# Optimization experiments

Hardware: AMD Instinct MI355X
Metric: run time of the kernel (lower is better)

The kernel has to match this reference:

```python
import jax, jax.numpy as jnp
import numpy as np

N, E, B = 100000, 1000000, 64
DIN, DS, H, NG = 128, 1024, 256, 20


def setup_inputs() -> dict:
    key = jax.random.key(0)
    ks = jax.random.split(key, 48)
    lin = lambda k, i, o: (jax.random.normal(k, (i, o), jnp.float32) / np.sqrt(i)).astype(jnp.float32)
    inp = {
        'x': jax.random.normal(ks[0], (N, DIN), jnp.float32),
        'edge_index': jax.random.randint(ks[1], (2, E), 0, N, jnp.int32),
        'batch': jnp.sort(jax.random.randint(ks[2], (N,), 0, B, jnp.int32)),
        'static_features': jax.random.normal(ks[3], (B, DS), jnp.float32),
        'temporal_feats': jax.random.normal(ks[4], (B, 5), jnp.float32),
        'type_idx': jax.random.randint(ks[5], (B,), 0, 10, jnp.int32),
        'type_emb': jax.random.normal(ks[6], (10, H), jnp.float32),
        # static encoder
        'Ws1': lin(ks[7], DS, H), 'bs1': jnp.zeros(H), 'Ws2': lin(ks[8], H, H), 'bs2': jnp.zeros(H),
        # 3 GCN convs
        'Wc1': lin(ks[9], DIN, H), 'bc1': jnp.zeros(H),
        'Wc2': lin(ks[10], H, H), 'bc2': jnp.zeros(H),
        'Wc3': lin(ks[11], H, H), 'bc3': jnp.zeros(H),
        # residual dim_match linears
        'Wd1': lin(ks[12], DIN, H), 'bd1': jnp.zeros(H),
        'Wd2': lin(ks[13], H, H), 'bd2': jnp.zeros(H),
        'Wd3': lin(ks[14], H, H), 'bd3': jnp.zeros(H),
        # temporal MLP (5 -> H//2 -> H)
        'Wt1': lin(ks[15], 5, H // 2), 'bt1': jnp.zeros(H // 2),
        'Wt2': lin(ks[16], H // 2, H), 'bt2': jnp.zeros(H),
        # pattern detector
        'Wp1': lin(ks[17], H, H // 2), 'bp1': jnp.zeros(H // 2),
        'Wp2': lin(ks[18], H // 2, H), 'bp2': jnp.zeros(H),
        # fusion (5H -> 2H -> H)
        'Wf1': lin(ks[19], 5 * H, 2 * H), 'bf1': jnp.zeros(2 * H),
        'Wf2': lin(ks[20], 2 * H, H), 'bf2': jnp.zeros(H),
        # heads
        'Wg': lin(ks[21], H, NG), 'bg': jnp.zeros(NG),
        'Wtp': lin(ks[22], H, 1), 'btp': jnp.zeros(1),
    }
    return inp


def reference(x, edge_index, batch, static_features, temporal_feats, type_idx, type_emb,
              Ws1, bs1, Ws2, bs2,
              Wc1, bc1, Wc2, bc2, Wc3, bc3,
              Wd1, bd1, Wd2, bd2, Wd3, bd3,
              Wt1, bt1, Wt2, bt2,
              Wp1, bp1, Wp2, bp2,
              Wf1, bf1, Wf2, bf2,
              Wg, bg, Wtp, btp):
    n = x.shape[0]
    b = static_features.shape[0]
    src, dst = edge_index[0], edge_index[1]
    # GCN symmetric norm with self-loops: deg = 1 + in-degree
    deg = 1.0 + jax.ops.segment_sum(jnp.ones(src.shape[0], x.dtype), dst, num_segments=n)
    dinv = deg ** -0.5
    ew = dinv[src] * dinv[dst]  # [E] edge norm weights

    def gcn(h_in, W, bias):
        h = h_in @ W  # [n, H]
        agg = jax.ops.segment_sum(h[src] * ew[:, None], dst, num_segments=n)
        return agg + h / deg[:, None] + bias  # neighbor agg + self-loop + bias

    # 3 GCN layers with residual dim_match (dropout is identity at inference)
    x1 = jax.nn.relu(gcn(x, Wc1, bc1)) + (x @ Wd1 + bd1)
    x2 = jax.nn.relu(gcn(x1, Wc2, bc2)) + (x1 @ Wd2 + bd2)
    x3 = jax.nn.relu(gcn(x2, Wc3, bc3)) + (x2 @ Wd3 + bd3)

    pat = jax.nn.relu(jax.nn.relu(x3 @ Wp1 + bp1) @ Wp2 + bp2)

    counts = jnp.maximum(jax.ops.segment_sum(jnp.ones(n, x.dtype), batch, num_segments=b), 1.0)
    graph_embed = jax.ops.segment_sum(x3, batch, num_segments=b) / counts[:, None]
    pattern_embed = jax.ops.segment_sum(pat, batch, num_segments=b) / counts[:, None]

    static_embed = jax.nn.relu(static_features @ Ws1 + bs1) @ Ws2 + bs2
    temporal_embed = jax.nn.relu(temporal_feats @ Wt1 + bt1) @ Wt2 + bt2
    type_embed = type_emb[type_idx]

    combined = jnp.concatenate([graph_embed, static_embed, temporal_embed, type_embed, pattern_embed], axis=1)
    fused = jax.nn.relu(combined @ Wf1 + bf1) @ Wf2 + bf2
    group_logits = fused @ Wg + bg
    time_pred = fused @ Wtp + btp
    return fused, group_logits, time_pred
```

## Files before the change

### kernel.cpp

```cpp
#include <hip/hip_runtime.h>

#define H 256
#define LDK 40

typedef __attribute__((ext_vector_type(8))) short bf16x8;
typedef __attribute__((ext_vector_type(4))) float f32x4;

__device__ __forceinline__ float b2f(ushort h) {
    return __uint_as_float(((unsigned)h) << 16);
}
__device__ __forceinline__ ushort f2bf(float f) {
    unsigned u = __float_as_uint(f);
    unsigned r = (u + 0x7FFF + ((u >> 16) & 1)) >> 16;
    return (ushort)r;
}

__global__ __launch_bounds__(256) void k_zero2_i(int* p, int* q, int n) {
    int i = blockIdx.x * 256 + threadIdx.x;
    if (i < n) { p[i] = 0; q[i] = 0; }
}

__global__ __launch_bounds__(256) void k_zero_f(float* p, int n) {
    int i = blockIdx.x * 256 + threadIdx.x;
    if (i < n) p[i] = 0.f;
}

__global__ __launch_bounds__(256) void k_count_deg_i(const int* __restrict__ dst, int* cnt, int E) {
    int i = blockIdx.x * 256 + threadIdx.x;
    if (i < E) atomicAdd(&cnt[dst[i]], 1);
}

__global__ __launch_bounds__(256) void k_scan1(const int* __restrict__ cnt, int* __restrict__ partial,
                                               int* __restrict__ bsums, int N) {
    __shared__ int s[256];
    int t = threadIdx.x;
    int idx = blockIdx.x * 256 + t;
    int v = idx < N ? cnt[idx] : 0;
    s[t] = v;
    __syncthreads();
    for (int off = 1; off < 256; off <<= 1) {
        int add = (t >= off) ? s[t - off] : 0;
        __syncthreads();
        s[t] += add;
        __syncthreads();
    }
    if (idx < N) partial[idx] = s[t];
    if (t == 255) bsums[blockIdx.x] = s[t];
}

__global__ __launch_bounds__(1024) void k_scan2(int* bsums, int nb) {
    __shared__ int s[1024];
    int t = threadIdx.x;
    s[t] = (t < nb) ? bsums[t] : 0;
    __syncthreads();
    for (int off = 1; off < 1024; off <<= 1) {
        int add = (t >= off) ? s[t - off] : 0;
        __syncthreads();
        s[t] += add;
        __syncthreads();
    }
    if (t < nb) bsums[t] = s[t];
}

__global__ __launch_bounds__(256) void k_scan3(const int* __restrict__ partial, const int* __restrict__ bsums,
                                               const int* __restrict__ cnt,
                                               int* __restrict__ rowptr, float* __restrict__ dinv,
                                               float* __restrict__ selfw, int N) {
    int idx = blockIdx.x * 256 + threadIdx.x;
    if (idx < N) {
        int off = blockIdx.x > 0 ? bsums[blockIdx.x - 1] : 0;
        rowptr[idx + 1] = partial[idx] + off;
        if (idx == 0) rowptr[0] = 0;
        float d = 1.0f + (float)cnt[idx];
        dinv[idx] = rsqrtf(d);
        selfw[idx] = 1.0f / d;
    }
}

__global__ __launch_bounds__(256) void k_scatter(const int* __restrict__ src, const int* __restrict__ dst,
                                                 const float* __restrict__ dinv, const int* __restrict__ rowptr,
                                                 int* __restrict__ fill, int* __restrict__ esrc,
                                                 float* __restrict__ ewt, int E) {
    int e = blockIdx.x * 256 + threadIdx.x;
    if (e >= E) return;
    int s = src[e], d = dst[e];
    int pos = rowptr[d] + atomicAdd(&fill[d], 1);
    esrc[pos] = s;
    ewt[pos] = dinv[s] * dinv[d];
}

__device__ __forceinline__ void tcvt_one(long i, const float* __restrict__ W, ushort* __restrict__ Wt,
                                         int K, int M) {
    int k = (int)(i / M), m = (int)(i - (long)k * M);
    Wt[(size_t)m * K + k] = f2bf(W[(size_t)k * M + m]);
}

__global__ __launch_bounds__(256) void k_prep(
    const float* __restrict__ x, ushort* __restrict__ xh, long nx, int DIN,
    const float* __restrict__ Wc1, ushort* Wc1t, const float* __restrict__ Wd1, ushort* Wd1t,
    const float* __restrict__ Wc2, ushort* Wc2t, const float* __restrict__ Wd2, ushort* Wd2t,
    const float* __restrict__ Wc3, ushort* Wc3t, const float* __restrict__ Wd3, ushort* Wd3t,
    const float* __restrict__ Wp1, ushort* Wp1t, const float* __restrict__ Wp2, ushort* Wp2t) {
    long i = (long)blockIdx.x * 256 + threadIdx.x;
    if (i < nx) { xh[i] = f2bf(x[i]); return; }
    i -= nx;
    long n1 = (long)DIN * 256;
    if (i < n1) { tcvt_one(i, Wc1, Wc1t, DIN, 256); return; }
    i -= n1;
    if (i < n1) { tcvt_one(i, Wd1, Wd1t, DIN, 256); return; }
    i -= n1;
    if (i < 65536) { tcvt_one(i, Wc2, Wc2t, 256, 256); return; }
    i -= 65536;
    if (i < 65536) { tcvt_one(i, Wd2, Wd2t, 256, 256); return; }
    i -= 65536;
    if (i < 65536) { tcvt_one(i, Wc3, Wc3t, 256, 256); return; }
    i -= 65536;
    if (i < 65536) { tcvt_one(i, Wd3, Wd3t, 256, 256); return; }
    i -= 65536;
    if (i < 32768) { tcvt_one(i, Wp1, Wp1t, 256, 128); return; }
    i -= 32768;
    if (i < 32768) { tcvt_one(i, Wp2, Wp2t, 128, 256); return; }
}

__global__ __launch_bounds__(256) void k_gather_b4(const ushort* __restrict__ xin, const int* __restrict__ rowptr,
                                                   const int* __restrict__ esrc, const float* __restrict__ ewt,
                                                   const float* __restrict__ selfw, ushort* __restrict__ p,
                                                   int N, int SX, int SP) {
    int node = blockIdx.x * 4 + (threadIdx.x >> 6);
    if (node >= N) return;
    int c = (threadIdx.x & 63) << 2;
    ushort4 h = *(const ushort4*)(xin + (size_t)node * SX + c);
    float sw = selfw[node];
    float a0 = b2f(h.x) * sw, a1 = b2f(h.y) * sw, a2 = b2f(h.z) * sw, a3 = b2f(h.w) * sw;
    int j = rowptr[node], r1 = rowptr[node + 1];
    for (; j + 3 < r1; j += 4) {
        int s0 = esrc[j], s1 = esrc[j + 1], s2 = esrc[j + 2], s3 = esrc[j + 3];
        float w0 = ewt[j], w1 = ewt[j + 1], w2 = ewt[j + 2], w3 = ewt[j + 3];
        ushort4 v0 = *(const ushort4*)(xin + (size_t)s0 * SX + c);
        ushort4 v1 = *(const ushort4*)(xin + (size_t)s1 * SX + c);
        ushort4 v2 = *(const ushort4*)(xin + (size_t)s2 * SX + c);
        ushort4 v3 = *(const ushort4*)(xin + (size_t)s3 * SX + c);
        a0 += b2f(v0.x) * w0 + b2f(v1.x) * w1 + b2f(v2.x) * w2 + b2f(v3.x) * w3;
        a1 += b2f(v0.y) * w0 + b2f(v1.y) * w1 + b2f(v2.y) * w2 + b2f(v3.y) * w3;
        a2 += b2f(v0.z) * w0 + b2f(v1.z) * w1 + b2f(v2.z) * w2 + b2f(v3.z) * w3;
        a3 += b2f(v0.w) * w0 + b2f(v1.w) * w1 + b2f(v2.w) * w2 + b2f(v3.w) * w3;
    }
    for (; j < r1; ++j) {
        int s0 = esrc[j];
        float w0 = ewt[j];
        ushort4 v0 = *(const ushort4*)(xin + (size_t)s0 * SX + c);
        a0 += b2f(v0.x) * w0; a1 += b2f(v0.y) * w0; a2 += b2f(v0.z) * w0; a3 += b2f(v0.w) * w0;
    }
    ushort4 o;
    o.x = f2bf(a0); o.y = f2bf(a1); o.z = f2bf(a2); o.w = f2bf(a3);
    *(ushort4*)(p + (size_t)node * SP + c) = o;
}

__global__ __launch_bounds__(256) void k_gather_b2(const ushort* __restrict__ xin, const int* __restrict__ rowptr,
                                                   const int* __restrict__ esrc, const float* __restrict__ ewt,
                                                   const float* __restrict__ selfw, ushort* __restrict__ p,
                                                   int N, int SX, int SP) {
    int node = blockIdx.x * 4 + (threadIdx.x >> 6);
    if (node >= N) return;
    int c = (threadIdx.x & 63) << 1;
    ushort2 h = *(const ushort2*)(xin + (size_t)node * SX + c);
    float sw = selfw[node];
    float a0 = b2f(h.x) * sw, a1 = b2f(h.y) * sw;
    int j = rowptr[node], r1 = rowptr[node + 1];
    for (; j + 3 < r1; j += 4) {
        int s0 = esrc[j], s1 = esrc[j + 1], s2 = esrc[j + 2], s3 = esrc[j + 3];
        float w0 = ewt[j], w1 = ewt[j + 1], w2 = ewt[j + 2], w3 = ewt[j + 3];
        ushort2 v0 = *(const ushort2*)(xin + (size_t)s0 * SX + c);
        ushort2 v1 = *(const ushort2*)(xin + (size_t)s1 * SX + c);
        ushort2 v2 = *(const ushort2*)(xin + (size_t)s2 * SX + c);
        ushort2 v3 = *(const ushort2*)(xin + (size_t)s3 * SX + c);
        a0 += b2f(v0.x) * w0 + b2f(v1.x) * w1 + b2f(v2.x) * w2 + b2f(v3.x) * w3;
        a1 += b2f(v0.y) * w0 + b2f(v1.y) * w1 + b2f(v2.y) * w2 + b2f(v3.y) * w3;
    }
    for (; j < r1; ++j) {
        int s0 = esrc[j];
        float w0 = ewt[j];
        ushort2 v0 = *(const ushort2*)(xin + (size_t)s0 * SX + c);
        a0 += b2f(v0.x) * w0; a1 += b2f(v0.y) * w0;
    }
    ushort2 o;
    o.x = f2bf(a0); o.y = f2bf(a1);
    *(ushort2*)(p + (size_t)node * SP + c) = o;
}

__global__ __launch_bounds__(256, 2) void k_fused_mfma(
    const ushort* __restrict__ Pm, const ushort* __restrict__ X,
    const ushort* __restrict__ Wct, const ushort* __restrict__ Wdt,
    const float* __restrict__ bc, const float* __restrict__ bd,
    ushort* __restrict__ Out, int N, int K, int SP, int SX) {
    __shared__ short Ps[64 * LDK];
    __shared__ short Xs[64 * LDK];
    __shared__ short Wcs[256 * LDK];
    __shared__ short Wds[256 * LDK];
    const int tid = threadIdx.x;
    const int wave = tid >> 6, lane = tid & 63;
    const int row0 = blockIdx.x * 64;

    f32x4 accC[4][4], accD[4][4];
#pragma unroll
    for (int i = 0; i < 4; ++i)
#pragma unroll
        for (int j = 0; j < 4; ++j) { accC[i][j] = (f32x4)0.f; accD[i][j] = (f32x4)0.f; }

    const int sr = tid >> 2, sc = (tid & 3) * 8;
    int grow = row0 + sr; if (grow > N - 1) grow = N - 1;
    const int m = lane & 15, kh = (lane >> 4) * 8;

    for (int k0 = 0; k0 < K; k0 += 32) {
        *(uint4*)&Ps[sr * LDK + sc] = *(const uint4*)(Pm + (size_t)grow * SP + k0 + sc);
        *(uint4*)&Xs[sr * LDK + sc] = *(const uint4*)(X + (size_t)grow * SX + k0 + sc);
#pragma unroll
        for (int p = 0; p < 4; ++p) {
            int col = p * 64 + (tid >> 2);
            *(uint4*)&Wcs[col * LDK + sc] = *(const uint4*)(Wct + (size_t)col * K + k0 + sc);
            *(uint4*)&Wds[col * LDK + sc] = *(const uint4*)(Wdt + (size_t)col * K + k0 + sc);
        }
        __syncthreads();
        bf16x8 aP[4], aX[4], bC[4], bD[4];
#pragma unroll
        for (int i = 0; i < 4; ++i) {
            aP[i] = *(bf16x8*)&Ps[(16 * i + m) * LDK + kh];
            aX[i] = *(bf16x8*)&Xs[(16 * i + m) * LDK + kh];
        }
#pragma unroll
        for (int j = 0; j < 4; ++j) {
            int c = wave * 64 + 16 * j + m;
            bC[j] = *(bf16x8*)&Wcs[c * LDK + kh];
            bD[j] = *(bf16x8*)&Wds[c * LDK + kh];
        }
#pragma unroll
        for (int i = 0; i < 4; ++i)
#pragma unroll
            for (int j = 0; j < 4; ++j) {
                accC[i][j] = __builtin_amdgcn_mfma_f32_16x16x32_bf16(aP[i], bC[j], accC[i][j], 0, 0, 0);
                accD[i][j] = __builtin_amdgcn_mfma_f32_16x16x32_bf16(aX[i], bD[j], accD[i][j], 0, 0, 0);
            }
        __syncthreads();
    }

    const int rq = (lane >> 4) * 4;
#pragma unroll
    for (int j = 0; j < 4; ++j) {
        int col = wave * 64 + 16 * j + m;
        float bcv = bc[col], bdv = bd[col];
#pragma unroll
        for (int i = 0; i < 4; ++i)
#pragma unroll
            for (int g = 0; g < 4; ++g) {
                int row = row0 + 16 * i + rq + g;
                if (row < N) {
                    float v = fmaxf(accC[i][j][g] + bcv, 0.f) + accD[i][j][g] + bdv;
                    Out[(size_t)row * 256 + col] = f2bf(v);
                }
            }
    }
}

__global__ __launch_bounds__(256, 2) void k_gemm_mfma(
    const ushort* __restrict__ A, const ushort* __restrict__ Wt, const float* __restrict__ bias,
    ushort* __restrict__ Out, int N, int K, int M, int SA, int dorelu) {
    __shared__ short As[128 * LDK];
    __shared__ short Wls[256 * LDK];
    const int tid = threadIdx.x;
    const int wave = tid >> 6, lane = tid & 63;
    const int MW = M >> 6;
    const int R = 16384 / M;
    const int row0 = blockIdx.x * R;
    const int row_off = (wave / MW) * 64, col_off = (wave % MW) * 64;

    f32x4 acc[4][4];
#pragma unroll
    for (int i = 0; i < 4; ++i)
#pragma unroll
        for (int j = 0; j < 4; ++j) acc[i][j] = (f32x4)0.f;

    const int m = lane & 15, kh = (lane >> 4) * 8, sc = (tid & 3) * 8;

    for (int k0 = 0; k0 < K; k0 += 32) {
        for (int c = tid; c < R * 4; c += 256) {
            int r = c >> 2, ck = (c & 3) * 8;
            int gr = row0 + r; if (gr > N - 1) gr = N - 1;
            *(uint4*)&As[r * LDK + ck] = *(const uint4*)(A + (size_t)gr * SA + k0 + ck);
        }
        for (int p = 0; p < MW; ++p) {
            int col = p * 64 + (tid >> 2);
            *(uint4*)&Wls[col * LDK + sc] = *(const uint4*)(Wt + (size_t)col * K + k0 + sc);
        }
        __syncthreads();
        bf16x8 af[4], bf[4];
#pragma unroll
        for (int i = 0; i < 4; ++i) af[i] = *(bf16x8*)&As[(row_off + 16 * i + m) * LDK + kh];
#pragma unroll
        for (int j = 0; j < 4; ++j) bf[j] = *(bf16x8*)&Wls[(col_off + 16 * j + m) * LDK + kh];
#pragma unroll
        for (int i = 0; i < 4; ++i)
#pragma unroll
            for (int j = 0; j < 4; ++j)
                acc[i][j] = __builtin_amdgcn_mfma_f32_16x16x32_bf16(af[i], bf[j], acc[i][j], 0, 0, 0);
        __syncthreads();
    }

    const int rq = (lane >> 4) * 4;
#pragma unroll
    for (int j = 0; j < 4; ++j) {
        int col = col_off + 16 * j + m;
        float bv = bias[col];
#pragma unroll
        for (int i = 0; i < 4; ++i)
#pragma unroll
            for (int g = 0; g < 4; ++g) {
                int row = row0 + row_off + 16 * i + rq + g;
                if (row < N) {
                    float v = acc[i][j][g] + bv;
                    if (dorelu) v = fmaxf(v, 0.f);
                    Out[(size_t)row * M + col] = f2bf(v);
                }
            }
    }
}

__global__ __launch_bounds__(256, 2) void k_pat2_pool(
    const ushort* __restrict__ A, const ushort* __restrict__ Wt, const float* __restrict__ bias,
    const int* __restrict__ batch, float* __restrict__ pesum, int N, int K, int SA) {
    __shared__ short As[64 * LDK];
    __shared__ short Wls[256 * LDK];
    __shared__ int sbatch[64];
    const int tid = threadIdx.x;
    const int wave = tid >> 6, lane = tid & 63;
    const int row0 = blockIdx.x * 64;
    const int col_off = wave * 64;

    f32x4 acc[4][4];
#pragma unroll
    for (int i = 0; i < 4; ++i)
#pragma unroll
        for (int j = 0; j < 4; ++j) acc[i][j] = (f32x4)0.f;

    const int m = lane & 15, kh = (lane >> 4) * 8, sc = (tid & 3) * 8;
    if (tid < 64) {
        int r = row0 + tid;
        sbatch[tid] = batch[r < N ? r : (N - 1)];
    }

    for (int k0 = 0; k0 < K; k0 += 32) {
        {
            int r = tid >> 2, ck = (tid & 3) * 8;
            int gr = row0 + r; if (gr > N - 1) gr = N - 1;
            *(uint4*)&As[r * LDK + ck] = *(const uint4*)(A + (size_t)gr * SA + k0 + ck);
        }
#pragma unroll
        for (int p = 0; p < 4; ++p) {
            int col = p * 64 + (tid >> 2);
            *(uint4*)&Wls[col * LDK + sc] = *(const uint4*)(Wt + (size_t)col * K + k0 + sc);
        }
        __syncthreads();
        bf16x8 af[4], bf[4];
#pragma unroll
        for (int i = 0; i < 4; ++i) af[i] = *(bf16x8*)&As[(16 * i + m) * LDK + kh];
#pragma unroll
        for (int j = 0; j < 4; ++j) bf[j] = *(bf16x8*)&Wls[(col_off + 16 * j + m) * LDK + kh];
#pragma unroll
        for (int i = 0; i < 4; ++i)
#pragma unroll
            for (int j = 0; j < 4; ++j)
                acc[i][j] = __builtin_amdgcn_mfma_f32_16x16x32_bf16(af[i], bf[j], acc[i][j], 0, 0, 0);
        __syncthreads();
    }

    const int rq = (lane >> 4) * 4;
    const int g0 = sbatch[0];
    const int g1 = sbatch[63];
    for (int g = g0; g <= g1; ++g) {
#pragma unroll
        for (int j = 0; j < 4; ++j) {
            float bv = bias[col_off + 16 * j + m];
            float s = 0.f;
#pragma unroll
            for (int i = 0; i < 4; ++i)
#pragma unroll
                for (int q = 0; q < 4; ++q) {
                    int rl = 16 * i + rq + q;
                    bool ok = (sbatch[rl] == g) && (row0 + rl < N);
                    float v = fmaxf(acc[i][j][q] + bv, 0.f);
                    s += ok ? v : 0.f;
                }
            s += __shfl_down(s, 32, 64);
            s += __shfl_down(s, 16, 64);
            if (lane < 16) atomicAdd(&pesum[(size_t)g * 256 + col_off + 16 * j + lane], s);
        }
    }
}

__global__ void k_ranges(const int* __restrict__ batch, int N, int B, int* __restrict__ start,
                         float* __restrict__ countsf) {
    int b = threadIdx.x;
    if (b <= B) {
        int lo = 0, hi = N;
        while (lo < hi) {
            int mid = (lo + hi) >> 1;
            if (batch[mid] < b) lo = mid + 1; else hi = mid;
        }
        start[b] = lo;
    }
    __syncthreads();
    if (b < B) {
        int cnt = start[b + 1] - start[b];
        countsf[b] = (float)(cnt > 0 ? cnt : 1);
    }
}

#define POOLS 16
__global__ __launch_bounds__(256) void k_pool2(const ushort* __restrict__ M_, const int* __restrict__ start,
                                               float* __restrict__ outsum) {
    int b = blockIdx.x;
    int s = blockIdx.y;
    int wave = threadIdx.x >> 6, lane = threadIdx.x & 63;
    int r0 = start[b], r1 = start[b + 1];
    int stripe = s * 4 + wave;
    float a0 = 0.f, a1 = 0.f, a2 = 0.f, a3 = 0.f;
    for (int r = r0 + stripe; r < r1; r += POOLS * 4) {
        ushort4 v = *(const ushort4*)(M_ + (size_t)r * 256 + lane * 4);
        a0 += b2f(v.x); a1 += b2f(v.y); a2 += b2f(v.z); a3 += b2f(v.w);
    }
    __shared__ float red[4][256];
    *(float4*)&red[wave][lane * 4] = make_float4(a0, a1, a2, a3);
    __syncthreads();
    int col = threadIdx.x;
    float t = red[0][col] + red[1][col] + red[2][col] + red[3][col];
    if (t != 0.f) atomicAdd(&outsum[(size_t)b * 256 + col], t);
}

__global__ __launch_bounds__(256) void k_fin_comb(const float* __restrict__ gesum, const float* __restrict__ pesum,
                                                  const float* __restrict__ countsf,
                                                  const float* __restrict__ temb, const int* __restrict__ tidx,
                                                  float* __restrict__ comb) {
    int b = blockIdx.x, t = threadIdx.x;
    float inv = 1.0f / countsf[b];
    float* o = comb + (size_t)b * 1280;
    o[t] = gesum[(size_t)b * 256 + t] * inv;
    o[768 + t] = temb[(size_t)tidx[b] * 256 + t];
    o[1024 + t] = pesum[(size_t)b * 256 + t] * inv;
}

__global__ __launch_bounds__(256) void k_dense(const float* __restrict__ vin, int vs,
                                               const float* __restrict__ W, const float* __restrict__ bias,
                                               float* __restrict__ out, int os, int oo,
                                               int K, int M, int relu) {
    const int b = blockIdx.y;
    const int wave = threadIdx.x >> 6, lane = threadIdx.x & 63;
    const int c = blockIdx.x * 64 + lane;
    const float* vrow = vin + (size_t)b * vs;
    float acc = 0.f;
    int k = wave;
    for (; k + 28 < K; k += 32) {
#pragma unroll
        for (int u = 0; u < 8; ++u)
            acc += vrow[k + 4 * u] * W[(size_t)(k + 4 * u) * M + c];
    }
    for (; k < K; k += 4)
        acc += vrow[k] * W[(size_t)k * M + c];
    __shared__ float red[4][64];
    red[wave][lane] = acc;
    __syncthreads();
    if (wave == 0) {
        float s = red[0][lane] + red[1][lane] + red[2][lane] + red[3][lane] + bias[c];
        if (relu) s = fmaxf(s, 0.f);
        out[(size_t)b * os + oo + c] = s;
    }
}

__global__ __launch_bounds__(256) void k_heads_small(const float* __restrict__ fused,
                                                     const float* __restrict__ Wg, const float* __restrict__ bg,
                                                     const float* __restrict__ Wtp, const float* __restrict__ btp,
                                                     float* __restrict__ out_logits, float* __restrict__ out_tp,
                                                     int NG) {
    __shared__ float lf[256];
    int b = blockIdx.x, tid = threadIdx.x;
    int wave = tid >> 6, lane = tid & 63;
    lf[tid] = fused[(size_t)b * 256 + tid];
    __syncthreads();
    for (int c = wave; c < NG; c += 4) {
        float s = 0.f;
#pragma unroll
        for (int k = lane; k < 256; k += 64) s += lf[k] * Wg[(size_t)k * NG + c];
#pragma unroll
        for (int off = 32; off > 0; off >>= 1) s += __shfl_down(s, off, 64);
        if (lane == 0) out_logits[(size_t)b * NG + c] = s + bg[c];
    }
    if (wave == 0) {
        float s = 0.f;
#pragma unroll
        for (int k = lane; k < 256; k += 64) s += lf[k] * Wtp[k];
#pragma unroll
        for (int off = 32; off > 0; off >>= 1) s += __shfl_down(s, off, 64);
        if (lane == 0) out_tp[b] = s + btp[0];
    }
}

extern "C" void kernel_launch(void* const* d_in, const int* in_sizes, int n_in,
                              void* d_out, int out_size, void* d_ws, size_t ws_size,
                              hipStream_t stream) {
    const float* x   = (const float*)d_in[0];
    const int* ei    = (const int*)d_in[1];
    const int* batch = (const int*)d_in[2];
    const float* sf  = (const float*)d_in[3];
    const float* tf  = (const float*)d_in[4];
    const int* tidx  = (const int*)d_in[5];
    const float* temb = (const float*)d_in[6];
    const float *Ws1 = (const float*)d_in[7],  *bs1 = (const float*)d_in[8];
    const float *Ws2 = (const float*)d_in[9],  *bs2 = (const float*)d_in[10];
    const float *Wc1 = (const float*)d_in[11], *bc1 = (const float*)d_in[12];
    const float *Wc2 = (const float*)d_in[13], *bc2 = (const float*)d_in[14];
    const float *Wc3 = (const float*)d_in[15], *bc3 = (const float*)d_in[16];
    const float *Wd1 = (const float*)d_in[17], *bd1 = (const float*)d_in[18];
    const float *Wd2 = (const float*)d_in[19], *bd2 = (const float*)d_in[20];
    const float *Wd3 = (const float*)d_in[21], *bd3 = (const float*)d_in[22];
    const float *Wt1 = (const float*)d_in[23], *bt1 = (const float*)d_in[24];
    const float *Wt2 = (const float*)d_in[25], *bt2 = (const float*)d_in[26];
    const float *Wp1 = (const float*)d_in[27], *bp1 = (const float*)d_in[28];
    const float *Wp2 = (const float*)d_in[29], *bp2 = (const float*)d_in[30];
    const float *Wf1 = (const float*)d_in[31], *bf1 = (const float*)d_in[32];
    const float *Wf2 = (const float*)d_in[33], *bf2 = (const float*)d_in[34];
    const float *Wg  = (const float*)d_in[35], *bg  = (const float*)d_in[36];
    const float *Wtp = (const float*)d_in[37], *btp = (const float*)d_in[38];

    const int N = in_sizes[2];
    const int E = in_sizes[1] / 2;
    const int B = in_sizes[5];
    const int DIN = in_sizes[0] / N;
    const int DS = in_sizes[3] / B;
    const int NG = in_sizes[36];
    const int* src = ei;
    const int* dst = ei + E;

    char* w = (char*)d_ws;
    ushort* A   = (ushort*)w;              w += (size_t)N * 256 * 2;
    ushort* Bb  = (ushort*)w;              w += (size_t)N * 256 * 2;
    ushort* xh  = (ushort*)w;              w += (size_t)N * 128 * 2;
    ushort* Wc1t = (ushort*)w;             w += 128 * 256 * 2;
    ushort* Wd1t = (ushort*)w;             w += 128 * 256 * 2;
    ushort* Wc2t = (ushort*)w;             w += 256 * 256 * 2;
    ushort* Wd2t = (ushort*)w;             w += 256 * 256 * 2;
    ushort* Wc3t = (ushort*)w;             w += 256 * 256 * 2;
    ushort* Wd3t = (ushort*)w;             w += 256 * 256 * 2;
    ushort* Wp1t = (ushort*)w;             w += 256 * 128 * 2;
    ushort* Wp2t = (ushort*)w;             w += 128 * 256 * 2;
    int* esrc   = (int*)w;                 w += (size_t)E * 4;
    float* ewt  = (float*)w;               w += (size_t)E * 4;
    int* cnt    = (int*)w;                 w += (size_t)N * 4;
    int* part   = (int*)w;                 w += (size_t)N * 4;
    int* rowptr = (int*)w;                 w += (size_t)(N + 1) * 4;
    int* fill   = (int*)w;                 w += (size_t)N * 4;
    int* bsums  = (int*)w;                 w += 1024 * 4;
    float* dinv = (float*)w;               w += (size_t)N * 4;
    float* selfw = (float*)w;              w += (size_t)N * 4;
    int* startp = (int*)w;                 w += (B + 1) * 4;
    float* countsf = (float*)w;            w += B * 4;
    float* ge = (float*)w;                 w += B * 256 * 4;
    float* pe = (float*)w;                 w += B * 256 * 4;
    float* s1buf = (float*)w;              w += B * 256 * 4;
    float* t1buf = (float*)w;              w += B * 128 * 4;
    float* comb = (float*)w;               w += B * 1280 * 4;
    float* fh = (float*)w;                 w += B * 512 * 4;

    float* out_fused = (float*)d_out;
    float* out_logits = out_fused + (size_t)B * H;
    float* out_tp = out_logits + (size_t)B * NG;

    dim3 blk(256);
    const int nbN = (N + 255) / 256;
    const int nbE = (E + 255) / 256;

    k_zero2_i<<<dim3(nbN), blk, 0, stream>>>(cnt, fill, N);
    k_count_deg_i<<<dim3(nbE), blk, 0, stream>>>(dst, cnt, E);
    k_scan1<<<dim3(nbN), blk, 0, stream>>>(cnt, part, bsums, N);
    k_scan2<<<dim3(1), dim3(1024), 0, stream>>>(bsums, nbN);
    k_scan3<<<dim3(nbN), blk, 0, stream>>>(part, bsums, cnt, rowptr, dinv, selfw, N);
    k_scatter<<<dim3(nbE), blk, 0, stream>>>(src, dst, dinv, rowptr, fill, esrc, ewt, E);

    {
        long nx = (long)N * DIN;
        long tot = nx + 2L * DIN * 256 + 4L * 65536 + 2L * 32768;
        k_prep<<<dim3((unsigned)((tot + 255) / 256)), blk, 0, stream>>>(
            x, xh, nx, DIN, Wc1, Wc1t, Wd1, Wd1t, Wc2, Wc2t, Wd2, Wd2t,
            Wc3, Wc3t, Wd3, Wd3t, Wp1, Wp1t, Wp2, Wp2t);
        k_ranges<<<dim3(1), dim3(128), 0, stream>>>(batch, N, B, startp, countsf);
        k_zero_f<<<dim3((2 * B * 256 + 255) / 256), blk, 0, stream>>>(ge, 2 * B * 256);
    }

    const int ngb = (N + 3) / 4;
    const int nfb = (N + 63) / 64;

    k_dense<<<dim3(4, B), blk, 0, stream>>>(sf, DS, Ws1, bs1, s1buf, 256, 0, DS, 256, 1);
    k_dense<<<dim3(4, B), blk, 0, stream>>>(s1buf, 256, Ws2, bs2, comb, 1280, 256, 256, 256, 0);
    k_dense<<<dim3(2, B), blk, 0, stream>>>(tf, 5, Wt1, bt1, t1buf, 128, 0, 5, 128, 1);
    k_dense<<<dim3(4, B), blk, 0, stream>>>(t1buf, 128, Wt2, bt2, comb, 1280, 512, 128, 256, 0);

    k_gather_b2<<<dim3(ngb), blk, 0, stream>>>(xh, rowptr, esrc, ewt, selfw, A, N, 128, 128);
    k_fused_mfma<<<dim3(nfb), blk, 0, stream>>>(A, xh, Wc1t, Wd1t, bc1, bd1, Bb, N, 128, 128, 128);
    k_gather_b4<<<dim3(ngb), blk, 0, stream>>>(Bb, rowptr, esrc, ewt, selfw, A, N, 256, 256);
    k_fused_mfma<<<dim3(nfb), blk, 0, stream>>>(A, Bb, Wc2t, Wd2t, bc2, bd2, A, N, 256, 256, 256);
    k_gather_b4<<<dim3(ngb), blk, 0, stream>>>(A, rowptr, esrc, ewt, selfw, Bb, N, 256, 256);
    k_fused_mfma<<<dim3(nfb), blk, 0, stream>>>(Bb, A, Wc3t, Wd3t, bc3, bd3, Bb, N, 256, 256, 256);

    k_pool2<<<dim3(B, POOLS), blk, 0, stream>>>(Bb, startp, ge);
    k_gemm_mfma<<<dim3((N + 127) / 128), blk, 0, stream>>>(Bb, Wp1t, bp1, A, N, 256, 128, 256, 1);
    k_pat2_pool<<<dim3((N + 63) / 64), blk, 0, stream>>>(A, Wp2t, bp2, batch, pe, N, 128, 128);
    k_fin_comb<<<dim3(B), blk, 0, stream>>>(ge, pe, countsf, temb, tidx, comb);

    k_dense<<<dim3(8, B), blk, 0, stream>>>(comb, 1280, Wf1, bf1, fh, 512, 0, 1280, 512, 1);
    k_dense<<<dim3(4, B), blk, 0, stream>>>(fh, 512, Wf2, bf2, out_fused, 256, 0, 512, 256, 0);
    k_heads_small<<<dim3(B), blk, 0, stream>>>(out_fused, Wg, bg, Wtp, btp, out_logits, out_tp, NG);
}
```

Measured before the change: 871.9 us.

## Use direct global-to-LDS loads with XOR swizzle and K=64 tiles in fused GCN GEMM

The fused conv+residual MFMA kernel now stages tiles with global_load_lds (buffer-to-LDS DMA) instead of loading through registers, doubles the K tile from 32 to 64, and replaces row padding with an XOR swizzle on the 16-byte chunk index to avoid LDS bank conflicts. This targets VGPR pressure and load/store instruction overhead in the staging phase and halves the number of barriers per K. LDS use rises to about 80KB per block, which may reduce occupancy below the two blocks per CU requested by the launch bounds. It also requires K to be a multiple of 64.

```diff
diff --git a/kernel.cpp b/kernel.cpp
--- a/kernel.cpp
+++ b/kernel.cpp
@@ -13,6 +13,12 @@
     unsigned u = __float_as_uint(f);
     unsigned r = (u + 0x7FFF + ((u >> 16) & 1)) >> 16;
     return (ushort)r;
+}
+
+__device__ __forceinline__ void gload16(const ushort* g, const short* l) {
+    __builtin_amdgcn_global_load_lds(
+        (const __attribute__((address_space(1))) void*)(const void*)g,
+        (__attribute__((address_space(3))) void*)(void*)l, 16, 0, 0);
 }
 
 __global__ __launch_bounds__(256) void k_zero2_i(int* p, int* q, int n) {
@@ -193,10 +199,10 @@
     const ushort* __restrict__ Wct, const ushort* __restrict__ Wdt,
     const float* __restrict__ bc, const float* __restrict__ bd,
     ushort* __restrict__ Out, int N, int K, int SP, int SX) {
-    __shared__ short Ps[64 * LDK];
-    __shared__ short Xs[64 * LDK];
-    __shared__ short Wcs[256 * LDK];
-    __shared__ short Wds[256 * LDK];
+    __shared__ __align__(16) short Ps[64 * 64];
+    __shared__ __align__(16) short Xs[64 * 64];
+    __shared__ __align__(16) short Wcs[256 * 64];
+    __shared__ __align__(16) short Wds[256 * 64];
     const int tid = threadIdx.x;
     const int wave = tid >> 6, lane = tid & 63;
     const int row0 = blockIdx.x * 64;
@@ -207,43 +213,57 @@
 #pragma unroll
         for (int j = 0; j < 4; ++j) { accC[i][j] = (f32x4)0.f; accD[i][j] = (f32x4)0.f; }
 
-    const int sr = tid >> 2, sc = (tid & 3) * 8;
-    int grow = row0 + sr; if (grow > N - 1) grow = N - 1;
-    const int m = lane & 15, kh = (lane >> 4) * 8;
-
-    for (int k0 = 0; k0 < K; k0 += 32) {
-        *(uint4*)&Ps[sr * LDK + sc] = *(const uint4*)(Pm + (size_t)grow * SP + k0 + sc);
-        *(uint4*)&Xs[sr * LDK + sc] = *(const uint4*)(X + (size_t)grow * SX + k0 + sc);
-#pragma unroll
-        for (int p = 0; p < 4; ++p) {
-            int col = p * 64 + (tid >> 2);
-            *(uint4*)&Wcs[col * LDK + sc] = *(const uint4*)(Wct + (size_t)col * K + k0 + sc);
-            *(uint4*)&Wds[col * LDK + sc] = *(const uint4*)(Wdt + (size_t)col * K + k0 + sc);
-        }
-        __syncthreads();
-        bf16x8 aP[4], aX[4], bC[4], bD[4];
-#pragma unroll
-        for (int i = 0; i < 4; ++i) {
-            aP[i] = *(bf16x8*)&Ps[(16 * i + m) * LDK + kh];
-            aX[i] = *(bf16x8*)&Xs[(16 * i + m) * LDK + kh];
-        }
-#pragma unroll
-        for (int j = 0; j < 4; ++j) {
-            int c = wave * 64 + 16 * j + m;
-            bC[j] = *(bf16x8*)&Wcs[c * LDK + kh];
-            bD[j] = *(bf16x8*)&Wds[c * LDK + kh];
-        }
-#pragma unroll
-        for (int i = 0; i < 4; ++i)
+    const int lr = lane >> 3;
+    const int ls = lane & 7;
+    const int swz = (ls ^ lr) << 3;
+    const int m = lane & 15, t4 = lane >> 4;
+
+    for (int k0 = 0; k0 < K; k0 += 64) {
+#pragma unroll
+        for (int i = 0; i < 2; ++i) {
+            int rr = wave * 16 + i * 8;
+            int gr = row0 + rr + lr; if (gr > N - 1) gr = N - 1;
+            gload16(Pm + (size_t)gr * SP + k0 + swz, &Ps[rr * 64]);
+            gload16(X + (size_t)gr * SX + k0 + swz, &Xs[rr * 64]);
+        }
+#pragma unroll
+        for (int i = 0; i < 8; ++i) {
+            int cc = wave * 64 + i * 8;
+            gload16(Wct + (size_t)(cc + lr) * K + k0 + swz, &Wcs[cc * 64]);
+            gload16(Wdt + (size_t)(cc + lr) * K + k0 + swz, &Wds[cc * 64]);
+        }
+        __syncthreads();
+
+#pragma unroll
+        for (int h = 0; h < 2; ++h) {
+            const int slot = h * 4 + t4;
+            bf16x8 aP[4], aX[4], bC[4], bD[4];
+#pragma unroll
+            for (int i = 0; i < 4; ++i) {
+                int r = 16 * i + m;
+                int off = r * 64 + ((slot ^ (r & 7)) << 3);
+                aP[i] = *(bf16x8*)&Ps[off];
+                aX[i] = *(bf16x8*)&Xs[off];
+            }
 #pragma unroll
             for (int j = 0; j < 4; ++j) {
-                accC[i][j] = __builtin_amdgcn_mfma_f32_16x16x32_bf16(aP[i], bC[j], accC[i][j], 0, 0, 0);
-                accD[i][j] = __builtin_amdgcn_mfma_f32_16x16x32_bf16(aX[i], bD[j], accD[i][j], 0, 0, 0);
+                int c = wave * 64 + 16 * j + m;
+                int off = c * 64 + ((slot ^ (c & 7)) << 3);
+                bC[j] = *(bf16x8*)&Wcs[off];
+                bD[j] = *(bf16x8*)&Wds[off];
             }
-        __syncthreads();
-    }
-
-    const int rq = (lane >> 4) * 4;
+#pragma unroll
+            for (int i = 0; i < 4; ++i)
+#pragma unroll
+                for (int j = 0; j < 4; ++j) {
+                    accC[i][j] = __builtin_amdgcn_mfma_f32_16x16x32_bf16(aP[i], bC[j], accC[i][j], 0, 0, 0);
+                    accD[i][j] = __builtin_amdgcn_mfma_f32_16x16x32_bf16(aX[i], bD[j], accD[i][j], 0, 0, 0);
+                }
+        }
+        __syncthreads();
+    }
+
+    const int rq = t4 * 4;
 #pragma unroll
     for (int j = 0; j < 4; ++j) {
         int col = wave * 64 + 16 * j + m;
```

Result: faster. 838.5 us (-3.8%).
